# Kernel optimization log

Measured on AMD Instinct MI355X. Metric: run time of the kernel, lower is better.

Reference implementation:

```python
import jax, jax.numpy as jnp
import numpy as np

B, M, H, D, C = 512, 40, 128, 64, 128


def setup_inputs() -> dict:
    key = jax.random.key(0)
    k1, k2, k3, k4 = jax.random.split(key, 4)
    x0 = jax.random.normal(k1, (B, M, D), dtype=jnp.float32)
    xk = jax.random.normal(k2, (B, H, D), dtype=jnp.float32)
    # Conv1d(kernel_size=1) weight [C, H*M, 1] squeezed to [C, H*M]; bias [C]
    W = jax.random.normal(k3, (C, H * M), dtype=jnp.float32) * 0.02
    b = jax.random.normal(k4, (C,), dtype=jnp.float32) * 0.02
    return {"x0": x0, "xk": xk, "W": W, "b": b}


def reference(x0, xk, W, b):
    # torch: outer[b, h*M+m, d] = xk[b,h,d] * x0[b,m,d]; out = conv1d(outer)
    # conv1d with kernel_size=1 is a channel contraction:
    #   out[b,c,d] = sum_{h,m} W[c, h*M+m] * xk[b,h,d] * x0[b,m,d] + b[c]
    Bsz, Hh, Dd = xk.shape
    Mm = x0.shape[1]
    Cc = W.shape[0]
    Wr = W.reshape(Cc, Hh, Mm)  # channel index is h*M + m -> [C, H, M]
    out = jnp.einsum('bhd,bmd,chm->bcd', xk, x0, Wr) + b[None, :, None]
    return out  # [B, C, D]
```

## Files before the change

### kernel.cpp

```cpp
#include <hip/hip_runtime.h>
#include <hip/hip_bf16.h>

typedef __attribute__((ext_vector_type(8))) short short8;
typedef __attribute__((ext_vector_type(4))) float f32x4;
typedef unsigned short u16;
typedef unsigned int u32;

#define NB 512
#define NM 40
#define NH 128
#define ND 64
#define NC 128
#define KTOT 5120

__device__ __forceinline__ u16 f2bf_rne(float f) {
    u32 u = __float_as_uint(f);
    u32 r = u + 0x7FFFu + ((u >> 16) & 1u);
    return (u16)(r >> 16);
}
__device__ __forceinline__ float bf2f(short s) {
    return __uint_as_float(((u32)(u16)s) << 16);
}

__device__ __forceinline__ short8 bmul(float s, short8 xv) {
    union { short8 s8; u32 u4[4]; } r;
#pragma unroll
    for (int j = 0; j < 4; ++j) {
        float f0 = s * bf2f(xv[2 * j]);
        float f1 = s * bf2f(xv[2 * j + 1]);
        r.u4[j] = __builtin_amdgcn_perm(__float_as_uint(f1), __float_as_uint(f0),
                                        0x07060302u);
    }
    return r.s8;
}

__global__ void w3_kernel(const float* __restrict__ W, u16* __restrict__ W3) {
    __shared__ u16 kbuf[KTOT];
    const int c = blockIdx.x;
    const float* src = W + (size_t)c * KTOT;
    for (int k = threadIdx.x; k < KTOT; k += 256)
        kbuf[k] = f2bf_rne(src[k]);
    __syncthreads();
    for (int n8 = threadIdx.x; n8 < 640; n8 += 256) {
        int m = n8 % 40, hh = n8 / 40;
        union { short8 s8; u16 e[8]; } v;
#pragma unroll
        for (int j = 0; j < 8; ++j)
            v.e[j] = kbuf[hh * 320 + j * 40 + m];
        int t = n8 >> 2, q = n8 & 3;
        *(short8*)(W3 + (size_t)t * 4096 + q * 1024 + c * 8) = v.s8;
    }
}

__global__ void __launch_bounds__(512, 2) cin_main(
    const float* __restrict__ x0g, const float* __restrict__ xkg,
    const float* __restrict__ biasg, const u16* __restrict__ W3,
    float* __restrict__ out)
{
    __shared__ __align__(16) char smem[135680];
    short* xkT    = (short*)smem;
    float* x0s    = (float*)(smem + 34816);
    float* bufA   = (float*)smem;
    float* bufB   = (float*)(smem + 67584);
    float* bias_s = (float*)(smem + 135168);

    const int tid = threadIdx.x;
    const int w = tid >> 6, L = tid & 63;
    const int q = L >> 4, l16 = L & 15;
    const int kh = w >> 1;
    const int rh = w & 1;
    const size_t b0 = 2 * (size_t)blockIdx.x;

    const u16* Ap = W3 + q * 1024 + (size_t)(rh * 64 + l16) * 8;
    auto loadA = [&](int t, short8* a) {
#pragma unroll
        for (int mt = 0; mt < 4; ++mt)
            a[mt] = *(const short8*)(Ap + (size_t)t * 4096 + mt * 128);
    };

    short8 aC[4], aN[4];
    const int t0 = kh * 40;
    loadA(t0, aC);

    {
        for (int i = tid; i < 4096; i += 512) {
            int bn = i >> 11, rem = i & 2047;
            int h = rem >> 4, d4 = (rem & 15) << 2;
            float4 v = *(const float4*)(xkg + (b0 + bn) * (NH * ND) + h * ND + d4);
            short* xT = xkT + bn * 8704;
            xT[(d4 + 0) * 136 + h] = (short)f2bf_rne(v.x);
            xT[(d4 + 1) * 136 + h] = (short)f2bf_rne(v.y);
            xT[(d4 + 2) * 136 + h] = (short)f2bf_rne(v.z);
            xT[(d4 + 3) * 136 + h] = (short)f2bf_rne(v.w);
        }
        for (int i = tid; i < 1280; i += 512) {
            int bn = i / 640, rem = i % 640;
            int m = rem >> 4, d4 = (rem & 15) << 2;
            *(f32x4*)(x0s + bn * 2720 + m * 68 + d4) =
                *(const f32x4*)(x0g + (b0 + bn) * (NM * ND) + m * ND + d4);
        }
        if (tid < NC) bias_s[tid] = biasg[tid];
    }
    __syncthreads();

    f32x4 acc[4][8] = {};
    short8 xv[8];

    for (int tp = 0; tp < 4; ++tp) {
        const int hh = kh * 4 + tp;
#pragma unroll
        for (int n = 0; n < 8; ++n) {
            const short* xT = xkT + (n >> 2) * 8704;
            xv[n] = *(const short8*)&xT[((n & 3) * 16 + l16) * 136 + hh * 8];
        }
#pragma unroll 2
        for (int ti = 0; ti < 10; ++ti) {
            const int tt = tp * 10 + ti;
            const int tn = (tt + 1 < 40) ? (t0 + tt + 1) : t0;
            loadA(tn, aN);
            const float* p0 = x0s + (4 * ti + q) * 68 + l16;
            const float* p1 = p0 + 2720;
#pragma unroll
            for (int n = 0; n < 8; ++n) {
                float s = (n < 4) ? p0[(n & 3) * 16] : p1[(n & 3) * 16];
                short8 bf = bmul(s, xv[n]);
                acc[0][n] = __builtin_amdgcn_mfma_f32_16x16x32_bf16(aC[0], bf, acc[0][n], 0, 0, 0);
                acc[1][n] = __builtin_amdgcn_mfma_f32_16x16x32_bf16(aC[1], bf, acc[1][n], 0, 0, 0);
                acc[2][n] = __builtin_amdgcn_mfma_f32_16x16x32_bf16(aC[2], bf, acc[2][n], 0, 0, 0);
                acc[3][n] = __builtin_amdgcn_mfma_f32_16x16x32_bf16(aC[3], bf, acc[3][n], 0, 0, 0);
            }
#pragma unroll
            for (int mt = 0; mt < 4; ++mt) aC[mt] = aN[mt];
        }
    }

    const int cbase = rh * 64 + q * 4;
    auto bufp = [&](float* buf, int mt, int n) -> float* {
        int d = (n & 3) * 16 + l16;
        return buf + (n >> 2) * 8448 + d * 132 + cbase + mt * 16;
    };
    __syncthreads();
    if (kh & 1) {
        float* buf = (kh == 1) ? bufA : bufB;
#pragma unroll
        for (int mt = 0; mt < 4; ++mt)
#pragma unroll
            for (int n = 0; n < 8; ++n)
                *(f32x4*)bufp(buf, mt, n) = acc[mt][n];
    }
    __syncthreads();
    if (!(kh & 1)) {
        float* buf = (kh == 0) ? bufA : bufB;
#pragma unroll
        for (int mt = 0; mt < 4; ++mt)
#pragma unroll
            for (int n = 0; n < 8; ++n)
                acc[mt][n] += *(const f32x4*)bufp(buf, mt, n);
    }
    __syncthreads();
    if (kh == 2) {
#pragma unroll
        for (int mt = 0; mt < 4; ++mt)
#pragma unroll
            for (int n = 0; n < 8; ++n)
                *(f32x4*)bufp(bufA, mt, n) = acc[mt][n];
    }
    __syncthreads();
    if (kh == 0) {
#pragma unroll
        for (int mt = 0; mt < 4; ++mt)
#pragma unroll
            for (int n = 0; n < 8; ++n) {
                acc[mt][n] += *(const f32x4*)bufp(bufA, mt, n);
                int bn = n >> 2, d = (n & 3) * 16 + l16;
                float* op = out + (b0 + bn) * (NC * ND);
#pragma unroll
                for (int rr = 0; rr < 4; ++rr) {
                    int c = cbase + mt * 16 + rr;
                    op[c * ND + d] = acc[mt][n][rr] + bias_s[c];
                }
            }
    }
}

extern "C" void kernel_launch(void* const* d_in, const int* in_sizes, int n_in,
                              void* d_out, int out_size, void* d_ws, size_t ws_size,
                              hipStream_t stream) {
    const float* x0 = (const float*)d_in[0];
    const float* xk = (const float*)d_in[1];
    const float* W  = (const float*)d_in[2];
    const float* bi = (const float*)d_in[3];
    float* out = (float*)d_out;

    u16* W3 = (u16*)d_ws;

    w3_kernel<<<NC, 256, 0, stream>>>(W, W3);
    cin_main<<<NB / 2, 512, 0, stream>>>(x0, xk, bi, W3, out);
}
```

Baseline: 123.5 us.

## Contract W with xk first and fold x0 via Abel-summation prefix accumulation

Reorders the contraction so MFMAs multiply the bf16 weights directly by the transposed xk tile, accumulating per-m partial sums T over h. The x0 scaling is applied by a summation-by-parts update o += (s_m - s_{m+1}) * T after each m, so T never has to be reset. This removes the per-MFMA VALU work that scaled and re-packed the B operand to bf16. The work split becomes batch/row/m-half, which needs only one shared-memory reduction stage and about half the LDS, possibly allowing higher occupancy. B fragments are now reloaded from LDS each step, the W3 layout changes to be m-major, and the prefix-sum formulation changes rounding behaviour.

```diff
diff --git a/kernel.cpp b/kernel.cpp
--- a/kernel.cpp
+++ b/kernel.cpp
@@ -18,21 +18,6 @@
     u32 r = u + 0x7FFFu + ((u >> 16) & 1u);
     return (u16)(r >> 16);
 }
-__device__ __forceinline__ float bf2f(short s) {
-    return __uint_as_float(((u32)(u16)s) << 16);
-}
-
-__device__ __forceinline__ short8 bmul(float s, short8 xv) {
-    union { short8 s8; u32 u4[4]; } r;
-#pragma unroll
-    for (int j = 0; j < 4; ++j) {
-        float f0 = s * bf2f(xv[2 * j]);
-        float f1 = s * bf2f(xv[2 * j + 1]);
-        r.u4[j] = __builtin_amdgcn_perm(__float_as_uint(f1), __float_as_uint(f0),
-                                        0x07060302u);
-    }
-    return r.s8;
-}
 
 __global__ void w3_kernel(const float* __restrict__ W, u16* __restrict__ W3) {
     __shared__ u16 kbuf[KTOT];
@@ -41,14 +26,13 @@
     for (int k = threadIdx.x; k < KTOT; k += 256)
         kbuf[k] = f2bf_rne(src[k]);
     __syncthreads();
-    for (int n8 = threadIdx.x; n8 < 640; n8 += 256) {
-        int m = n8 % 40, hh = n8 / 40;
+    for (int n = threadIdx.x; n < 640; n += 256) {
+        int m = n >> 4, t = (n >> 2) & 3, q = n & 3;
         union { short8 s8; u16 e[8]; } v;
 #pragma unroll
         for (int j = 0; j < 8; ++j)
-            v.e[j] = kbuf[hh * 320 + j * 40 + m];
-        int t = n8 >> 2, q = n8 & 3;
-        *(short8*)(W3 + (size_t)t * 4096 + q * 1024 + c * 8) = v.s8;
+            v.e[j] = kbuf[(t * 32 + q * 8 + j) * NM + m];
+        *(short8*)(W3 + ((size_t)n * 128 + c) * 8) = v.s8;
     }
 }
 
@@ -57,30 +41,27 @@
     const float* __restrict__ biasg, const u16* __restrict__ W3,
     float* __restrict__ out)
 {
-    __shared__ __align__(16) char smem[135680];
+    __shared__ __align__(16) char smem[70144];
     short* xkT    = (short*)smem;
     float* x0s    = (float*)(smem + 34816);
-    float* bufA   = (float*)smem;
-    float* bufB   = (float*)(smem + 67584);
-    float* bias_s = (float*)(smem + 135168);
+    float* red    = (float*)smem;
+    float* bias_s = (float*)(smem + 69632);
 
     const int tid = threadIdx.x;
     const int w = tid >> 6, L = tid & 63;
     const int q = L >> 4, l16 = L & 15;
-    const int kh = w >> 1;
-    const int rh = w & 1;
+    const int bh = (w >> 2) & 1;
+    const int rh = (w >> 1) & 1;
+    const int mh = w & 1;
     const size_t b0 = 2 * (size_t)blockIdx.x;
 
     const u16* Ap = W3 + q * 1024 + (size_t)(rh * 64 + l16) * 8;
-    auto loadA = [&](int t, short8* a) {
+    const int m0 = mh * 20;
+
+    short8 aC[4], aN[4], bC[4], bN[4];
 #pragma unroll
-        for (int mt = 0; mt < 4; ++mt)
-            a[mt] = *(const short8*)(Ap + (size_t)t * 4096 + mt * 128);
-    };
-
-    short8 aC[4], aN[4];
-    const int t0 = kh * 40;
-    loadA(t0, aC);
+    for (int mt = 0; mt < 4; ++mt)
+        aN[mt] = *(const short8*)(Ap + (size_t)m0 * 16384 + mt * 128);
 
     {
         for (int i = tid; i < 4096; i += 512) {
@@ -103,81 +84,83 @@
     }
     __syncthreads();
 
-    f32x4 acc[4][8] = {};
-    short8 xv[8];
+    const short* xT = xkT + bh * 8704;
+    const float* x0p = x0s + bh * 2720;
+    const short* Bp = xT + (size_t)l16 * 136 + q * 8;
+#pragma unroll
+    for (int n = 0; n < 4; ++n)
+        bN[n] = *(const short8*)(Bp + n * (16 * 136));
 
-    for (int tp = 0; tp < 4; ++tp) {
-        const int hh = kh * 4 + tp;
+    float s[4], sn[4];
 #pragma unroll
-        for (int n = 0; n < 8; ++n) {
-            const short* xT = xkT + (n >> 2) * 8704;
-            xv[n] = *(const short8*)&xT[((n & 3) * 16 + l16) * 136 + hh * 8];
-        }
-#pragma unroll 2
-        for (int ti = 0; ti < 10; ++ti) {
-            const int tt = tp * 10 + ti;
-            const int tn = (tt + 1 < 40) ? (t0 + tt + 1) : t0;
-            loadA(tn, aN);
-            const float* p0 = x0s + (4 * ti + q) * 68 + l16;
-            const float* p1 = p0 + 2720;
+    for (int n = 0; n < 4; ++n)
+        s[n] = x0p[m0 * 68 + n * 16 + l16];
+
+    f32x4 T[4][4] = {};
+    f32x4 o[4][4] = {};
+
+    for (int mi = 0; mi < 20; ++mi) {
+        const int m = m0 + mi;
+        const int mnext = (mi < 19) ? m + 1 : m;
 #pragma unroll
-            for (int n = 0; n < 8; ++n) {
-                float s = (n < 4) ? p0[(n & 3) * 16] : p1[(n & 3) * 16];
-                short8 bf = bmul(s, xv[n]);
-                acc[0][n] = __builtin_amdgcn_mfma_f32_16x16x32_bf16(aC[0], bf, acc[0][n], 0, 0, 0);
-                acc[1][n] = __builtin_amdgcn_mfma_f32_16x16x32_bf16(aC[1], bf, acc[1][n], 0, 0, 0);
-                acc[2][n] = __builtin_amdgcn_mfma_f32_16x16x32_bf16(aC[2], bf, acc[2][n], 0, 0, 0);
-                acc[3][n] = __builtin_amdgcn_mfma_f32_16x16x32_bf16(aC[3], bf, acc[3][n], 0, 0, 0);
+        for (int t = 0; t < 4; ++t) {
+#pragma unroll
+            for (int i2 = 0; i2 < 4; ++i2) { aC[i2] = aN[i2]; bC[i2] = bN[i2]; }
+            const int tn = (t + 1) & 3;
+            const size_t mA = (t < 3) ? (size_t)m : (size_t)mnext;
+#pragma unroll
+            for (int mt = 0; mt < 4; ++mt)
+                aN[mt] = *(const short8*)(Ap + mA * 16384 + tn * 4096 + mt * 128);
+#pragma unroll
+            for (int n = 0; n < 4; ++n)
+                bN[n] = *(const short8*)(Bp + n * (16 * 136) + tn * 32);
+            if (t == 0) {
+#pragma unroll
+                for (int n = 0; n < 4; ++n)
+                    sn[n] = (mi < 19) ? x0p[(m + 1) * 68 + n * 16 + l16] : 0.f;
             }
 #pragma unroll
-            for (int mt = 0; mt < 4; ++mt) aC[mt] = aN[mt];
+            for (int n = 0; n < 4; ++n) {
+                T[0][n] = __builtin_amdgcn_mfma_f32_16x16x32_bf16(aC[0], bC[n], T[0][n], 0, 0, 0);
+                T[1][n] = __builtin_amdgcn_mfma_f32_16x16x32_bf16(aC[1], bC[n], T[1][n], 0, 0, 0);
+                T[2][n] = __builtin_amdgcn_mfma_f32_16x16x32_bf16(aC[2], bC[n], T[2][n], 0, 0, 0);
+                T[3][n] = __builtin_amdgcn_mfma_f32_16x16x32_bf16(aC[3], bC[n], T[3][n], 0, 0, 0);
+            }
+        }
+#pragma unroll
+        for (int n = 0; n < 4; ++n) {
+            const float dd = s[n] - sn[n];
+#pragma unroll
+            for (int mt = 0; mt < 4; ++mt)
+                o[mt][n] += dd * T[mt][n];
+            s[n] = sn[n];
         }
     }
 
-    const int cbase = rh * 64 + q * 4;
-    auto bufp = [&](float* buf, int mt, int n) -> float* {
-        int d = (n & 3) * 16 + l16;
-        return buf + (n >> 2) * 8448 + d * 132 + cbase + mt * 16;
-    };
     __syncthreads();
-    if (kh & 1) {
-        float* buf = (kh == 1) ? bufA : bufB;
+    float* myred = red + (bh * 2 + rh) * 4352;
+    if (mh == 1) {
 #pragma unroll
         for (int mt = 0; mt < 4; ++mt)
 #pragma unroll
-            for (int n = 0; n < 8; ++n)
-                *(f32x4*)bufp(buf, mt, n) = acc[mt][n];
+            for (int n = 0; n < 4; ++n) {
+                int d = n * 16 + l16;
+                *(f32x4*)(myred + d * 68 + mt * 16 + q * 4) = o[mt][n];
+            }
     }
     __syncthreads();
-    if (!(kh & 1)) {
-        float* buf = (kh == 0) ? bufA : bufB;
+    if (mh == 0) {
+        float* op = out + (b0 + bh) * (NC * ND);
 #pragma unroll
         for (int mt = 0; mt < 4; ++mt)
 #pragma unroll
-            for (int n = 0; n < 8; ++n)
-                acc[mt][n] += *(const f32x4*)bufp(buf, mt, n);
-    }
-    __syncthreads();
-    if (kh == 2) {
-#pragma unroll
-        for (int mt = 0; mt < 4; ++mt)
-#pragma unroll
-            for (int n = 0; n < 8; ++n)
-                *(f32x4*)bufp(bufA, mt, n) = acc[mt][n];
-    }
-    __syncthreads();
-    if (kh == 0) {
-#pragma unroll
-        for (int mt = 0; mt < 4; ++mt)
-#pragma unroll
-            for (int n = 0; n < 8; ++n) {
-                acc[mt][n] += *(const f32x4*)bufp(bufA, mt, n);
-                int bn = n >> 2, d = (n & 3) * 16 + l16;
-                float* op = out + (b0 + bn) * (NC * ND);
+            for (int n = 0; n < 4; ++n) {
+                int d = n * 16 + l16;
+                f32x4 r = *(const f32x4*)(myred + d * 68 + mt * 16 + q * 4);
 #pragma unroll
                 for (int rr = 0; rr < 4; ++rr) {
-                    int c = cbase + mt * 16 + rr;
-                    op[c * ND + d] = acc[mt][n][rr] + bias_s[c];
+                    int c = rh * 64 + mt * 16 + q * 4 + rr;
+                    op[c * ND + d] = o[mt][n][rr] + r[rr] + bias_s[c];
                 }
             }
     }
```

After: 117.3 us. 5.0% less time.
